# Optimization experiments

Hardware: AMD Instinct MI355X
Metric: run time of the kernel (lower is better)

Reference implementation:

```python
import jax, jax.numpy as jnp
import numpy as np

F_BINS = 12
T_STEPS = 15
N = F_BINS * T_STEPS  # 180 patches
C = 768
R = C // 4            # 192 reduced dim for Q/K
B = 256
LN_EPS = 1e-5


def _build_physical_adjacency():
    A = np.zeros((N, N), dtype=np.float32)
    for f in range(F_BINS):
        for t in range(T_STEPS):
            i = f * T_STEPS + t
            if t < T_STEPS - 1:
                j = f * T_STEPS + (t + 1)
                A[i, j] = 1.0
                A[j, i] = 1.0
            hf = f * 2 + 1
            if hf < F_BINS:
                j = hf * T_STEPS + t
                A[i, j] = 1.0
                A[j, i] = 1.0
    A = A / (A.sum(axis=1, keepdims=True) + 1e-8)
    return jnp.asarray(A)


def setup_inputs() -> dict:
    key = jax.random.key(0)
    ks = jax.random.split(key, 8)
    x = jax.random.normal(ks[0], (B, N, C), dtype=jnp.float32)
    Wq = jax.random.normal(ks[1], (C, R), dtype=jnp.float32) * 0.02
    bq = jnp.zeros((R,), dtype=jnp.float32)
    Wk = jax.random.normal(ks[2], (C, R), dtype=jnp.float32) * 0.02
    bk = jnp.zeros((R,), dtype=jnp.float32)
    Wg = jax.random.normal(ks[3], (C, C), dtype=jnp.float32) * 0.02
    bg = jnp.zeros((C,), dtype=jnp.float32)
    gamma = jnp.ones((C,), dtype=jnp.float32)
    beta = jnp.zeros((C,), dtype=jnp.float32)
    alpha = jnp.asarray(0.8, dtype=jnp.float32)
    A_phys = _build_physical_adjacency()
    return {"x": x, "Wq": Wq, "bq": bq, "Wk": Wk, "bk": bk,
            "Wg": Wg, "bg": bg, "gamma": gamma, "beta": beta,
            "alpha": alpha, "A_phys": A_phys}


def reference(x, Wq, bq, Wk, bk, Wg, bg, gamma, beta, alpha, A_phys):
    # Q/K projections: [B,N,R]
    Q = jnp.einsum('bnc,cr->bnr', x, Wq) + bq
    K = jnp.einsum('bnc,cr->bnr', x, Wk) + bk
    # Dynamic adjacency: scaled dot-product softmax over nodes.
    scores = jnp.einsum('bnr,bmr->bnm', Q, K) / jnp.sqrt(jnp.asarray(R, x.dtype))
    A_dyn = jax.nn.softmax(scores, axis=-1)  # dropout is identity in eval
    a = jax.nn.sigmoid(alpha)
    A_comb = a * A_phys[None, :, :] + (1.0 - a) * A_dyn
    # GCN aggregation + projection
    z = jnp.einsum('bnm,bmc->bnc', A_comb, x)
    z = jnp.einsum('bnc,cd->bnd', z, Wg) + bg
    h = x + jax.nn.relu(z)
    # LayerNorm over channel dim
    mu = jnp.mean(h, axis=-1, keepdims=True)
    var = jnp.mean((h - mu) ** 2, axis=-1, keepdims=True)
    out = (h - mu) * jax.lax.rsqrt(var + LN_EPS) * gamma + beta
    return out
```

## Files before the change

kernel.cpp:

```cpp
#include <hip/hip_runtime.h>
#include <hip/hip_bf16.h>
#include <math.h>
#include <stdint.h>

#define BB   256
#define NN   180
#define CC   768
#define RR   192
#define MROWS (BB*NN)
#define KPAD 192

typedef __attribute__((ext_vector_type(8))) __bf16 bf16x8;
typedef __attribute__((ext_vector_type(4))) __bf16 bf16x4;
typedef __attribute__((ext_vector_type(4))) float  floatx4;

__device__ __forceinline__ void gload_lds16(const __bf16* g, __bf16* lds)
{
    __builtin_amdgcn_global_load_lds(
        (const __attribute__((address_space(1))) void*)(uintptr_t)(const void*)g,
        (__attribute__((address_space(3))) void*)(uintptr_t)(void*)lds,
        16, 0, 0);
}

template<int MODE>
__global__ __launch_bounds__(256) void gemm128(
    const __bf16* __restrict__ A,  int lda, long sAb,
    const __bf16* __restrict__ Bt, int ldb, long sBb,
    void* __restrict__ Cout, int ldc, long sCb,
    int M, int N, int K,
    const float* __restrict__ bias,
    const float* __restrict__ scale,
    const float* __restrict__ addx)
{
    const int z = blockIdx.z;
    const __bf16* Ab = A  + (long)z * sAb;
    const __bf16* Bb = Bt + (long)z * sBb;

    const int nwg = gridDim.x * gridDim.y;
    const int lin = blockIdx.y * gridDim.x + blockIdx.x;
    const int qd = nwg >> 3, rr = nwg & 7, xc = lin & 7, oo = lin >> 3;
    const int wg = (xc < rr ? xc * (qd + 1) : rr * (qd + 1) + (xc - rr) * qd) + oo;
    const int m0 = (wg / gridDim.x) * 128;
    const int n0 = (wg % gridDim.x) * 128;

    const int t  = threadIdx.x;
    const int w  = t >> 6;
    const int l  = t & 63;
    const int lr = l & 15;
    const int q  = l >> 4;
    const int xr = (lr >> 1) & 3;

    __shared__ __align__(16) __bf16 sa[3][128 * 32];
    __shared__ __align__(16) __bf16 sb[3][128 * 32];

    floatx4 acc[4][4] = {};

    const int wm = (w & 1) * 64;
    const int wn = (w >> 1) * 64;

    const int srow = l >> 2;
    const int skc  = ((l & 3) ^ ((l >> 3) & 3)) * 8;

    int arow0 = m0 + w * 16 + srow;        if (arow0 > M - 1) arow0 = M - 1;
    int arow1 = m0 + (w + 4) * 16 + srow;  if (arow1 > M - 1) arow1 = M - 1;
    int brow0 = n0 + w * 16 + srow;        if (brow0 > N - 1) brow0 = N - 1;
    int brow1 = n0 + (w + 4) * 16 + srow;  if (brow1 > N - 1) brow1 = N - 1;

    const __bf16* agp0 = Ab + (long)arow0 * lda + skc;
    const __bf16* agp1 = Ab + (long)arow1 * lda + skc;
    const __bf16* bgp0 = Bb + (long)brow0 * ldb + skc;
    const __bf16* bgp1 = Bb + (long)brow1 * ldb + skc;

    auto issue = [&](int slot, int cc) {
        const int k0 = cc * 32;
        gload_lds16(agp0 + k0, &sa[slot][(size_t)w * 512]);
        gload_lds16(agp1 + k0, &sa[slot][(size_t)(w + 4) * 512]);
        gload_lds16(bgp0 + k0, &sb[slot][(size_t)w * 512]);
        gload_lds16(bgp1 + k0, &sb[slot][(size_t)(w + 4) * 512]);
    };

    auto compute = [&](int slot) {
        bf16x8 af[4], bfv[4];
#pragma unroll
        for (int i = 0; i < 4; ++i)
            af[i] = *reinterpret_cast<const bf16x8*>(
                &sa[slot][(wm + i * 16 + lr) * 32 + ((q ^ xr) * 8)]);
#pragma unroll
        for (int j = 0; j < 4; ++j)
            bfv[j] = *reinterpret_cast<const bf16x8*>(
                &sb[slot][(wn + j * 16 + lr) * 32 + ((q ^ xr) * 8)]);
#pragma unroll
        for (int i = 0; i < 4; ++i)
#pragma unroll
            for (int j = 0; j < 4; ++j)
                acc[i][j] = __builtin_amdgcn_mfma_f32_16x16x32_bf16(af[i], bfv[j], acc[i][j], 0, 0, 0);
    };

    const int NC = K >> 5;

    issue(0, 0);
    issue(1, 1);
    asm volatile("s_waitcnt vmcnt(4)" ::: "memory");
    __builtin_amdgcn_sched_barrier(0);
    __builtin_amdgcn_s_barrier();
    __builtin_amdgcn_sched_barrier(0);

#pragma unroll 3
    for (int c = 0; c < NC; ++c) {
        const int cs = c % 3;
        if (c + 2 < NC) issue((c + 2) % 3, c + 2);
        compute(cs);
        if (c + 1 < NC) {
            if (c + 2 < NC) asm volatile("s_waitcnt vmcnt(4)" ::: "memory");
            else            asm volatile("s_waitcnt vmcnt(0)" ::: "memory");
            __builtin_amdgcn_sched_barrier(0);
            __builtin_amdgcn_s_barrier();
            __builtin_amdgcn_sched_barrier(0);
        }
    }

#pragma unroll
    for (int i = 0; i < 4; ++i) {
        const int mbase = m0 + wm + i * 16 + q * 4;
#pragma unroll
        for (int j = 0; j < 4; ++j) {
            const int n = n0 + wn + j * 16 + lr;
#pragma unroll
            for (int r = 0; r < 4; ++r) {
                const int m = mbase + r;
                if (m < M && n < N) {
                    float v = acc[i][j][r];
                    if (MODE == 0) {
                        v = (v + bias[n]) * scale[n];
                        ((__bf16*)Cout)[(long)z * sCb + (long)m * ldc + n] = (__bf16)v;
                    } else if (MODE == 1) {
                        ((__bf16*)Cout)[(long)z * sCb + (long)m * ldc + n] = (__bf16)v;
                    } else {
                        v = v + bias[n];
                        v = v > 0.f ? v : 0.f;
                        v += addx[(long)m * ldc + n];
                        ((float*)Cout)[(long)m * ldc + n] = v;
                    }
                }
            }
        }
    }
}

__global__ __launch_bounds__(256) void convert_transpose_x(
    const float* __restrict__ x, __bf16* __restrict__ xb, __bf16* __restrict__ xbT)
{
    const int c0 = (blockIdx.x % 12) * 64;
    const int b  = blockIdx.x / 12;
    __shared__ __bf16 lds[64 * 194];
    const int t = threadIdx.x;

    for (int i = 0; i < 12; ++i) {
        int idx = i * 256 + t;
        if (idx < 2880) {
            int m = idx >> 4, c4 = idx & 15;
            float4 v = *reinterpret_cast<const float4*>(
                &x[((long)(b * NN + m)) * CC + c0 + c4 * 4]);
            bf16x4 o;
            o[0] = (__bf16)v.x; o[1] = (__bf16)v.y;
            o[2] = (__bf16)v.z; o[3] = (__bf16)v.w;
            *reinterpret_cast<bf16x4*>(&xb[((long)(b * NN + m)) * CC + c0 + c4 * 4]) = o;
            lds[(c4 * 4 + 0) * 194 + m] = o[0];
            lds[(c4 * 4 + 1) * 194 + m] = o[1];
            lds[(c4 * 4 + 2) * 194 + m] = o[2];
            lds[(c4 * 4 + 3) * 194 + m] = o[3];
        }
    }
    __syncthreads();
    for (int j = 0; j < 48; ++j) {
        int idx = j * 256 + t;
        int c = idx / KPAD, m = idx % KPAD;
        __bf16 v = (m < NN) ? lds[c * 194 + m] : (__bf16)0.0f;
        xbT[((long)(b * CC + c0 + c)) * KPAD + m] = v;
    }
}

__global__ __launch_bounds__(256) void prep_weights(
    const float* __restrict__ Wq, const float* __restrict__ bq,
    const float* __restrict__ Wk, const float* __restrict__ bk,
    const float* __restrict__ Wg,
    __bf16* __restrict__ WqkT, __bf16* __restrict__ WgT,
    float* __restrict__ biasqk, float* __restrict__ scaleqk)
{
    int blk = blockIdx.x, t = threadIdx.x;
    if (blk < 384) {
        int n = blk;
        const float* W = (n < RR) ? Wq : Wk;
        int nn = (n < RR) ? n : n - RR;
        for (int k = t; k < CC; k += 256)
            WqkT[(long)n * CC + k] = (__bf16)W[(long)k * RR + nn];
        if (blk == 0) {
            for (int i = t; i < 384; i += 256) {
                biasqk[i]  = (i < RR) ? bq[i] : bk[i - RR];
                scaleqk[i] = (i < RR) ? rsqrtf((float)RR) : 1.0f;
            }
        }
    } else {
        int n = blk - 384;
        for (int k = t; k < CC; k += 256)
            WgT[(long)n * CC + k] = (__bf16)Wg[(long)k * CC + n];
    }
}

__global__ __launch_bounds__(256) void softmax_combine(
    const __bf16* __restrict__ S, const float* __restrict__ A_phys,
    const float* __restrict__ alpha, __bf16* __restrict__ Acomb)
{
    const int w = threadIdx.x >> 6, l = threadIdx.x & 63;
    const long row = (long)blockIdx.x * 4 + w;
    const int b = (int)(row / NN), n = (int)(row % NN);
    const __bf16* Srow = S + ((long)b * NN + n) * NN;

    float v[3];
#pragma unroll
    for (int i = 0; i < 3; ++i) {
        int m = l + 64 * i;
        v[i] = (m < NN) ? (float)Srow[m] : -1e30f;
    }
    float mx = fmaxf(fmaxf(v[0], v[1]), v[2]);
    for (int off = 32; off; off >>= 1) mx = fmaxf(mx, __shfl_xor(mx, off, 64));

    float e[3], sum = 0.f;
#pragma unroll
    for (int i = 0; i < 3; ++i) {
        int m = l + 64 * i;
        e[i] = (m < NN) ? expf(v[i] - mx) : 0.f;
        sum += e[i];
    }
    for (int off = 32; off; off >>= 1) sum += __shfl_xor(sum, off, 64);

    const float a   = 1.f / (1.f + expf(-alpha[0]));
    const float inv = (1.f - a) / sum;
    __bf16* Orow = Acomb + ((long)b * NN + n) * KPAD;
#pragma unroll
    for (int i = 0; i < 3; ++i) {
        int m = l + 64 * i;
        if (m < KPAD) {
            float o = (m < NN) ? (a * A_phys[n * NN + m] + e[i] * inv) : 0.f;
            Orow[m] = (__bf16)o;
        }
    }
}

__global__ __launch_bounds__(256) void ln_kernel(float* __restrict__ out,
                                                 const float* __restrict__ gamma,
                                                 const float* __restrict__ beta)
{
    float* p = out + (long)blockIdx.x * CC;
    const int t = threadIdx.x, w = t >> 6, l = t & 63;
    float h[3], s = 0.f, s2 = 0.f;
#pragma unroll
    for (int i = 0; i < 3; ++i) {
        h[i] = p[t + 256 * i];
        s += h[i]; s2 += h[i] * h[i];
    }
    for (int off = 32; off; off >>= 1) { s += __shfl_xor(s, off, 64); s2 += __shfl_xor(s2, off, 64); }
    __shared__ float ps[4], ps2[4];
    if (l == 0) { ps[w] = s; ps2[w] = s2; }
    __syncthreads();
    s  = ps[0] + ps[1] + ps[2] + ps[3];
    s2 = ps2[0] + ps2[1] + ps2[2] + ps2[3];
    const float mu  = s * (1.f / CC);
    const float var = s2 * (1.f / CC) - mu * mu;
    const float rs  = rsqrtf(var + 1e-5f);
#pragma unroll
    for (int i = 0; i < 3; ++i) {
        int c = t + 256 * i;
        p[c] = (h[i] - mu) * rs * gamma[c] + beta[c];
    }
}

extern "C" void kernel_launch(void* const* d_in, const int* in_sizes, int n_in,
                              void* d_out, int out_size, void* d_ws, size_t ws_size,
                              hipStream_t stream)
{
    const float* x      = (const float*)d_in[0];
    const float* Wq     = (const float*)d_in[1];
    const float* bq     = (const float*)d_in[2];
    const float* Wk     = (const float*)d_in[3];
    const float* bk     = (const float*)d_in[4];
    const float* Wg     = (const float*)d_in[5];
    const float* bg     = (const float*)d_in[6];
    const float* gamma  = (const float*)d_in[7];
    const float* beta   = (const float*)d_in[8];
    const float* alpha  = (const float*)d_in[9];
    const float* A_phys = (const float*)d_in[10];

    char* w = (char*)d_ws;
    __bf16* xb    = (__bf16*)(w + 0);
    __bf16* zbuf  = xb;
    __bf16* xbT   = (__bf16*)(w + 70778880);
    __bf16* QK    = (__bf16*)(w + 146276352);
    __bf16* Acomb = QK;
    __bf16* S     = (__bf16*)(w + 181665792);
    __bf16* WqkT  = (__bf16*)(w + 198254592);
    __bf16* WgT   = (__bf16*)(w + 198844416);
    float*  biasqk  = (float*)(w + 200024064);
    float*  scaleqk = (float*)(w + 200025600);

    prep_weights<<<384 + CC, 256, 0, stream>>>(Wq, bq, Wk, bk, Wg, WqkT, WgT, biasqk, scaleqk);
    convert_transpose_x<<<BB * 12, 256, 0, stream>>>(x, xb, xbT);

    gemm128<0><<<dim3(384 / 128, MROWS / 128, 1), 256, 0, stream>>>(
        xb, CC, 0L, WqkT, CC, 0L, QK, 384, 0L,
        MROWS, 384, CC, biasqk, scaleqk, nullptr);

    gemm128<1><<<dim3(2, 2, BB), 256, 0, stream>>>(
        QK, 384, (long)NN * 384, QK + RR, 384, (long)NN * 384,
        S, NN, (long)NN * NN,
        NN, NN, RR, nullptr, nullptr, nullptr);

    softmax_combine<<<MROWS / 4, 256, 0, stream>>>(S, A_phys, alpha, Acomb);

    gemm128<1><<<dim3(CC / 128, 2, BB), 256, 0, stream>>>(
        Acomb, KPAD, (long)NN * KPAD, xbT, KPAD, (long)CC * KPAD,
        zbuf, CC, (long)NN * CC,
        NN, CC, KPAD, nullptr, nullptr, nullptr);

    gemm128<3><<<dim3(CC / 128, MROWS / 128, 1), 256, 0, stream>>>(
        zbuf, CC, 0L, WgT, CC, 0L, d_out, CC, 0L,
        MROWS, CC, CC, bg, nullptr, x);

    ln_kernel<<<MROWS, 256, 0, stream>>>((float*)d_out, gamma, beta);
}
```

Measured before the change: 666.5 us.

## Use 256x128 tiled GEMM with triple-buffered LDS for the two large projections

Adds a gemm256m kernel with a 256-row by 128-column tile, where each wave computes a 128x64 block (8x4 MFMA tiles), backed by a three-stage LDS ring in dynamic shared memory. The kernel replaces the 128x128 GEMM for the QK projection and for the Wg projection with its fused bias/ReLU/residual epilogue. The larger tile raises operand reuse per LDS load and cuts redundant global reads of the B matrix. In exchange it needs more registers and 72KB of LDS, capped at 2 blocks per CU, and launches fewer workgroups. The M bound checks are dropped, which relies on M being a multiple of 256 (46080 is).

```diff
diff --git a/kernel.cpp b/kernel.cpp
--- a/kernel.cpp
+++ b/kernel.cpp
@@ -20,6 +20,127 @@
         (const __attribute__((address_space(1))) void*)(uintptr_t)(const void*)g,
         (__attribute__((address_space(3))) void*)(uintptr_t)(void*)lds,
         16, 0, 0);
+}
+
+template<int MODE>
+__global__ __launch_bounds__(256, 2) void gemm256m(
+    const __bf16* __restrict__ A,  int lda,
+    const __bf16* __restrict__ Bt, int ldb,
+    void* __restrict__ Cout, int ldc,
+    int M, int N, int K,
+    const float* __restrict__ bias,
+    const float* __restrict__ scale,
+    const float* __restrict__ addx)
+{
+    extern __shared__ __align__(16) __bf16 smem[];
+    __bf16 (*sa)[256 * 32] = (__bf16 (*)[256 * 32])(smem);
+    __bf16 (*sb)[128 * 32] = (__bf16 (*)[128 * 32])(smem + 3 * 8192);
+
+    const int nwg = gridDim.x * gridDim.y;
+    const int lin = blockIdx.y * gridDim.x + blockIdx.x;
+    const int qd = nwg >> 3, rr = nwg & 7, xc = lin & 7, oo = lin >> 3;
+    const int wg = (xc < rr ? xc * (qd + 1) : rr * (qd + 1) + (xc - rr) * qd) + oo;
+    const int m0 = (wg / gridDim.x) * 256;
+    const int n0 = (wg % gridDim.x) * 128;
+
+    const int t  = threadIdx.x;
+    const int w  = t >> 6;
+    const int l  = t & 63;
+    const int lr = l & 15;
+    const int q  = l >> 4;
+    const int xr = (lr >> 1) & 3;
+
+    floatx4 acc[8][4] = {};
+
+    const int wm = (w >> 1) * 128;
+    const int wn = (w & 1) * 64;
+
+    const int srow = l >> 2;
+    const int skc  = ((l & 3) ^ ((l >> 3) & 3)) * 8;
+
+    const __bf16* agp[4];
+#pragma unroll
+    for (int c = 0; c < 4; ++c)
+        agp[c] = A + (long)(m0 + c * 64 + w * 16 + srow) * lda + skc;
+    const __bf16* bgp[2];
+#pragma unroll
+    for (int c = 0; c < 2; ++c)
+        bgp[c] = Bt + (long)(n0 + c * 64 + w * 16 + srow) * ldb + skc;
+
+    auto issue = [&](int slot, int cc) {
+        const int k0 = cc * 32;
+#pragma unroll
+        for (int c = 0; c < 4; ++c)
+            gload_lds16(agp[c] + k0, &sa[slot][(size_t)(c * 4 + w) * 512]);
+#pragma unroll
+        for (int c = 0; c < 2; ++c)
+            gload_lds16(bgp[c] + k0, &sb[slot][(size_t)(c * 4 + w) * 512]);
+    };
+
+    auto compute = [&](int slot) {
+        bf16x8 af[8], bfv[4];
+#pragma unroll
+        for (int i = 0; i < 8; ++i)
+            af[i] = *reinterpret_cast<const bf16x8*>(
+                &sa[slot][(wm + i * 16 + lr) * 32 + ((q ^ xr) * 8)]);
+#pragma unroll
+        for (int j = 0; j < 4; ++j)
+            bfv[j] = *reinterpret_cast<const bf16x8*>(
+                &sb[slot][(wn + j * 16 + lr) * 32 + ((q ^ xr) * 8)]);
+#pragma unroll
+        for (int i = 0; i < 8; ++i)
+#pragma unroll
+            for (int j = 0; j < 4; ++j)
+                acc[i][j] = __builtin_amdgcn_mfma_f32_16x16x32_bf16(af[i], bfv[j], acc[i][j], 0, 0, 0);
+    };
+
+    const int NC = K >> 5;
+
+    issue(0, 0);
+    issue(1, 1);
+    asm volatile("s_waitcnt vmcnt(6)" ::: "memory");
+    __builtin_amdgcn_sched_barrier(0);
+    __builtin_amdgcn_s_barrier();
+    __builtin_amdgcn_sched_barrier(0);
+
+#pragma unroll 3
+    for (int c = 0; c < NC; ++c) {
+        const int cs = c % 3;
+        if (c + 2 < NC) issue((c + 2) % 3, c + 2);
+        compute(cs);
+        if (c + 1 < NC) {
+            if (c + 2 < NC) asm volatile("s_waitcnt vmcnt(6)" ::: "memory");
+            else            asm volatile("s_waitcnt vmcnt(0)" ::: "memory");
+            __builtin_amdgcn_sched_barrier(0);
+            __builtin_amdgcn_s_barrier();
+            __builtin_amdgcn_sched_barrier(0);
+        }
+    }
+
+#pragma unroll
+    for (int j = 0; j < 4; ++j) {
+        const int n = n0 + wn + j * 16 + lr;
+        const float bi = bias[n];
+        const float sc = (MODE == 0) ? scale[n] : 1.0f;
+#pragma unroll
+        for (int i = 0; i < 8; ++i) {
+            const int mbase = m0 + wm + i * 16 + q * 4;
+#pragma unroll
+            for (int r = 0; r < 4; ++r) {
+                const int m = mbase + r;
+                float v = acc[i][j][r];
+                if (MODE == 0) {
+                    v = (v + bi) * sc;
+                    ((__bf16*)Cout)[(long)m * ldc + n] = (__bf16)v;
+                } else {
+                    v = v + bi;
+                    v = v > 0.f ? v : 0.f;
+                    v += addx[(long)m * ldc + n];
+                    ((float*)Cout)[(long)m * ldc + n] = v;
+                }
+            }
+        }
+    }
 }
 
 template<int MODE>
@@ -130,17 +251,7 @@
                 const int m = mbase + r;
                 if (m < M && n < N) {
                     float v = acc[i][j][r];
-                    if (MODE == 0) {
-                        v = (v + bias[n]) * scale[n];
-                        ((__bf16*)Cout)[(long)z * sCb + (long)m * ldc + n] = (__bf16)v;
-                    } else if (MODE == 1) {
-                        ((__bf16*)Cout)[(long)z * sCb + (long)m * ldc + n] = (__bf16)v;
-                    } else {
-                        v = v + bias[n];
-                        v = v > 0.f ? v : 0.f;
-                        v += addx[(long)m * ldc + n];
-                        ((float*)Cout)[(long)m * ldc + n] = v;
-                    }
+                    ((__bf16*)Cout)[(long)z * sCb + (long)m * ldc + n] = (__bf16)v;
                 }
             }
         }
@@ -291,6 +402,15 @@
     const float* alpha  = (const float*)d_in[9];
     const float* A_phys = (const float*)d_in[10];
 
+    static bool attr_done = false;
+    if (!attr_done) {
+        auto k0 = gemm256m<0>;
+        auto k3 = gemm256m<3>;
+        hipFuncSetAttribute((const void*)k0, hipFuncAttributeMaxDynamicSharedMemorySize, 73728);
+        hipFuncSetAttribute((const void*)k3, hipFuncAttributeMaxDynamicSharedMemorySize, 73728);
+        attr_done = true;
+    }
+
     char* w = (char*)d_ws;
     __bf16* xb    = (__bf16*)(w + 0);
     __bf16* zbuf  = xb;
@@ -306,8 +426,8 @@
     prep_weights<<<384 + CC, 256, 0, stream>>>(Wq, bq, Wk, bk, Wg, WqkT, WgT, biasqk, scaleqk);
     convert_transpose_x<<<BB * 12, 256, 0, stream>>>(x, xb, xbT);
 
-    gemm128<0><<<dim3(384 / 128, MROWS / 128, 1), 256, 0, stream>>>(
-        xb, CC, 0L, WqkT, CC, 0L, QK, 384, 0L,
+    gemm256m<0><<<dim3(384 / 128, MROWS / 256, 1), 256, 73728, stream>>>(
+        xb, CC, WqkT, CC, QK, 384,
         MROWS, 384, CC, biasqk, scaleqk, nullptr);
 
     gemm128<1><<<dim3(2, 2, BB), 256, 0, stream>>>(
@@ -322,8 +442,8 @@
         zbuf, CC, (long)NN * CC,
         NN, CC, KPAD, nullptr, nullptr, nullptr);
 
-    gemm128<3><<<dim3(CC / 128, MROWS / 128, 1), 256, 0, stream>>>(
-        zbuf, CC, 0L, WgT, CC, 0L, d_out, CC, 0L,
+    gemm256m<3><<<dim3(CC / 128, MROWS / 256, 1), 256, 73728, stream>>>(
+        zbuf, CC, WgT, CC, d_out, CC,
         MROWS, CC, CC, bg, nullptr, x);
 
     ln_kernel<<<MROWS, 256, 0, stream>>>((float*)d_out, gamma, beta);
```

Measured after the change: 700.0 us. 1.05x slower.
